# Kernel tuning notes

Measured on AMD Instinct MI355X. Metric: run time of the kernel, lower is better.

The kernel has to match this reference:

```python
import jax, jax.numpy as jnp
import numpy as np

B, C, S = 64, 512, 768          # batch, num_channels(seq), spatial_dim
K, K_NEXT, A, H = 128, 256, 200, 1024  # num_classes, next_num_classes, attention_unit, fc_hidden
BN_EPS = 1e-5


def setup_inputs() -> dict:
    key = jax.random.key(0)
    ks = jax.random.split(key, 8)
    return {
        "x": jax.random.normal(ks[0], (B, C, S), dtype=jnp.float32),
        "omega_h": jax.random.normal(ks[1], (B, K, A), dtype=jnp.float32),
        "W_s1": jax.random.normal(ks[2], (A, S), dtype=jnp.float32) * 0.1,
        "W_s2": jax.random.normal(ks[3], (K, A), dtype=jnp.float32) * 0.1,
        "W_t": jax.random.normal(ks[4], (H, 2 * S), dtype=jnp.float32) * 0.1,
        "b_t": jnp.full((H,), 0.1, dtype=jnp.float32),
        "gamma": jnp.ones((H,), dtype=jnp.float32),
        "beta": jnp.zeros((H,), dtype=jnp.float32),
        "W_l": jax.random.normal(ks[5], (K, H), dtype=jnp.float32) * 0.1,
        "b_l": jnp.full((K,), 0.1, dtype=jnp.float32),
        "G_h": jax.random.normal(ks[6], (K, K_NEXT), dtype=jnp.float32) * 0.1,
    }


def reference(x, omega_h, W_s1, W_s2, W_t, b_t, gamma, beta, W_l, b_l, G_h):
    # --- TCCA ---
    # tanh(W_s1 @ x^T): [B, A, C]
    t = jnp.tanh(jnp.einsum('as,bcs->bac', W_s1, x))
    # (W_s2 * omega_h) @ t : [B, K, C]
    attn = jnp.einsum('bka,bac->bkc', W_s2 * omega_h, t)
    attn_w = jax.nn.softmax(attn, axis=1)  # softmax over class dim (dim=1), as in source
    attn_out = jnp.einsum('bkc,bcs->bks', attn_w, x)
    attn_out_avg = jnp.mean(attn_out, axis=1)  # [B, S]

    # --- HAM concat ---
    x_mean = jnp.mean(x, axis=1)  # [B, S]
    local_input = jnp.concatenate([x_mean, attn_out_avg], axis=1)  # [B, 2S]

    # --- CPM: linear -> batchnorm(train) -> relu -> linear -> sigmoid ---
    fc = local_input @ W_t.T + b_t  # [B, H]
    mu = jnp.mean(fc, axis=0)
    var = jnp.mean(jnp.square(fc - mu), axis=0)  # biased variance (torch BN normalization)
    fc_bn = (fc - mu) * jax.lax.rsqrt(var + BN_EPS) * gamma + beta
    local_fc_out = jax.nn.relu(fc_bn)
    local_score = jax.nn.sigmoid(local_fc_out @ W_l.T + b_l)  # [B, K]

    # --- CDM ---
    Q_h = local_score @ G_h  # [B, K_NEXT]
    omega_h_next = jnp.broadcast_to(Q_h[:, :, None], (B, K_NEXT, A))

    return (local_score, local_fc_out, omega_h_next)
```

## Files before the change

kernel.cpp:

```cpp
#include <hip/hip_runtime.h>
#include <math.h>

#define B_  64
#define C_  512
#define S_  768
#define K_  128
#define KN_ 256
#define A_  200
#define H_  1024

#define OUT_FC     8192
#define OUT_OMEGA  73728

#define SCR_WEFF   0
#define SCR_XMT    786432
#define SCR_FCRT   835584
#define SCR_SCORET 901120

__global__ void __launch_bounds__(256) kA(const float* __restrict__ Wt,
                                          float* __restrict__ weff,
                                          const float* __restrict__ x,
                                          float* __restrict__ xmT) {
    __shared__ float4 smem[256];
    int tid = threadIdx.x;
    if (blockIdx.x < 768) {
        int idx = blockIdx.x * 256 + tid;
        int h   = idx / 192;
        int s4  = idx - h * 192;
        const float4* a = (const float4*)(Wt + (size_t)h * 1536) + s4;
        const float4* b = (const float4*)(Wt + (size_t)h * 1536 + 768) + s4;
        float4 va = *a, vb = *b;
        float4 r;
        r.x = va.x + 4.0f * vb.x;
        r.y = va.y + 4.0f * vb.y;
        r.z = va.z + 4.0f * vb.z;
        r.w = va.w + 4.0f * vb.w;
        ((float4*)weff)[idx] = r;
    } else {
        int bid = blockIdx.x - 768;
        int b   = bid / 12;
        int st  = (bid - b * 12) * 64;
        int s4  = tid & 15;
        int cs  = tid >> 4;
        const float4* xb = (const float4*)(x + (size_t)b * C_ * S_);
        int col = (st >> 2) + s4;
        float4 acc = {0.f, 0.f, 0.f, 0.f};
        #pragma unroll 8
        for (int c = cs; c < C_; c += 16) {
            float4 v = xb[c * 192 + col];
            acc.x += v.x; acc.y += v.y; acc.z += v.z; acc.w += v.w;
        }
        smem[tid] = acc;
        __syncthreads();
        #pragma unroll
        for (int str = 8; str >= 1; str >>= 1) {
            if (cs < str) {
                float4 o = smem[tid + str * 16];
                float4 m = smem[tid];
                m.x += o.x; m.y += o.y; m.z += o.z; m.w += o.w;
                smem[tid] = m;
            }
            __syncthreads();
        }
        if (cs == 0) {
            float4 m = smem[tid];
            const float inv = 1.0f / (float)C_;
            int scol = st + s4 * 4;
            xmT[(scol + 0) * 64 + b] = m.x * inv;
            xmT[(scol + 1) * 64 + b] = m.y * inv;
            xmT[(scol + 2) * 64 + b] = m.z * inv;
            xmT[(scol + 3) * 64 + b] = m.w * inv;
        }
    }
}

__global__ void __launch_bounds__(256) kB(const float* __restrict__ xmT,
                                          const float* __restrict__ weff,
                                          const float* __restrict__ bt,
                                          const float* __restrict__ gamma,
                                          const float* __restrict__ beta,
                                          float* __restrict__ fcrT,
                                          float* __restrict__ out_fc) {
    int lane = threadIdx.x & 63;
    int h = __builtin_amdgcn_readfirstlane((blockIdx.x << 2) + (threadIdx.x >> 6));
    const float4* w4 = (const float4*)(weff + (size_t)h * S_);
    float acc = 0.f;
    #pragma unroll 4
    for (int s4 = 0; s4 < 192; ++s4) {
        float4 w = w4[s4];
        int s = s4 * 4;
        acc += xmT[(s + 0) * 64 + lane] * w.x
             + xmT[(s + 1) * 64 + lane] * w.y
             + xmT[(s + 2) * 64 + lane] * w.z
             + xmT[(s + 3) * 64 + lane] * w.w;
    }
    float v = acc + bt[h];
    float s1 = v, s2 = v * v;
    #pragma unroll
    for (int m = 1; m < 64; m <<= 1) {
        s1 += __shfl_xor(s1, m);
        s2 += __shfl_xor(s2, m);
    }
    float mu  = s1 * (1.0f / 64.0f);
    float var = s2 * (1.0f / 64.0f) - mu * mu;
    float r = (v - mu) * rsqrtf(var + 1e-5f) * gamma[h] + beta[h];
    r = fmaxf(r, 0.0f);
    fcrT[h * 64 + lane]   = r;
    out_fc[lane * H_ + h] = r;
}

__global__ void __launch_bounds__(256) kC(const float* __restrict__ fcrT,
                                          const float* __restrict__ Wl,
                                          const float* __restrict__ bl,
                                          float* __restrict__ scoreT,
                                          float* __restrict__ out_score) {
    __shared__ float sm[256];
    int tid  = threadIdx.x;
    int lane = tid & 63;
    int w    = tid >> 6;
    int k    = blockIdx.x;
    const float* wl = Wl + (size_t)k * H_ + w * 256;
    const float* f  = fcrT + (size_t)w * 256 * 64;
    float acc = 0.f;
    #pragma unroll 8
    for (int h = 0; h < 256; ++h)
        acc += f[h * 64 + lane] * wl[h];
    sm[tid] = acc;
    __syncthreads();
    if (tid < 64) {
        float t = sm[tid] + sm[64 + tid] + sm[128 + tid] + sm[192 + tid] + bl[k];
        float sc = 1.0f / (1.0f + expf(-t));
        scoreT[k * 64 + tid]    = sc;
        out_score[tid * K_ + k] = sc;
    }
}

__global__ void __launch_bounds__(256) kD(const float* __restrict__ scoreT,
                                          const float* __restrict__ Gh,
                                          float4* __restrict__ outO) {
    __shared__ float qh[KN_];
    int tid = threadIdx.x;
    int b   = blockIdx.x >> 2;
    int q   = blockIdx.x & 3;
    float acc = 0.f;
    #pragma unroll 8
    for (int k = 0; k < K_; ++k)
        acc += scoreT[k * 64 + b] * Gh[k * KN_ + tid];
    qh[tid] = acc;
    __syncthreads();
    float4* dst = outO + (size_t)b * 12800;
    int end = q * 3200 + 3200;
    for (int i = q * 3200 + tid; i < end; i += 256) {
        float v = qh[i / 50];
        float4 r; r.x = v; r.y = v; r.z = v; r.w = v;
        dst[i] = r;
    }
}

extern "C" void kernel_launch(void* const* d_in, const int* in_sizes, int n_in,
                              void* d_out, int out_size, void* d_ws, size_t ws_size,
                              hipStream_t stream) {
    const float* x     = (const float*)d_in[0];
    const float* Wt    = (const float*)d_in[4];
    const float* bt    = (const float*)d_in[5];
    const float* gamma = (const float*)d_in[6];
    const float* beta  = (const float*)d_in[7];
    const float* Wl    = (const float*)d_in[8];
    const float* bl    = (const float*)d_in[9];
    const float* Gh    = (const float*)d_in[10];

    float* out    = (float*)d_out;
    float* ws     = (float*)d_ws;
    float* weff   = ws + SCR_WEFF;
    float* xmT    = ws + SCR_XMT;
    float* fcrT   = ws + SCR_FCRT;
    float* scoreT = ws + SCR_SCORET;

    kA<<<1536, 256, 0, stream>>>(Wt, weff, x, xmT);
    kB<<<256,  256, 0, stream>>>(xmT, weff, bt, gamma, beta, fcrT, out + OUT_FC);
    kC<<<128,  256, 0, stream>>>(fcrT, Wl, bl, scoreT, out);
    kD<<<256,  256, 0, stream>>>(scoreT, Gh, (float4*)(out + OUT_OMEGA));
}
```

Measured before the change: 219.5 us.

## Fuse weight folding into FC kernel and split reductions across more waves

The precomputed folded weight buffer (Wa + 4·Wb) is dropped. The FC kernel now reads both halves of W_t directly and combines them inline, which removes a full write and re-read of the folded weights from scratch memory along with the extra blocks in the first kernel. The FC kernel splits each hidden unit's reduction over the spatial dimension across two waves and merges them through shared memory. The score kernel moves to 512 threads so each wave handles a shorter slice of H. The cost is more raw W_t bytes read inside the FC kernel and an extra block barrier.

```diff
diff --git a/kernel.cpp b/kernel.cpp
--- a/kernel.cpp
+++ b/kernel.cpp
@@ -12,123 +12,119 @@
 #define OUT_FC     8192
 #define OUT_OMEGA  73728
 
-#define SCR_WEFF   0
-#define SCR_XMT    786432
-#define SCR_FCRT   835584
-#define SCR_SCORET 901120
+#define SCR_XMT    0
+#define SCR_FCRT   49152
+#define SCR_SCORET 114688
 
-__global__ void __launch_bounds__(256) kA(const float* __restrict__ Wt,
-                                          float* __restrict__ weff,
-                                          const float* __restrict__ x,
+__global__ void __launch_bounds__(256) kA(const float* __restrict__ x,
                                           float* __restrict__ xmT) {
     __shared__ float4 smem[256];
     int tid = threadIdx.x;
-    if (blockIdx.x < 768) {
-        int idx = blockIdx.x * 256 + tid;
-        int h   = idx / 192;
-        int s4  = idx - h * 192;
-        const float4* a = (const float4*)(Wt + (size_t)h * 1536) + s4;
-        const float4* b = (const float4*)(Wt + (size_t)h * 1536 + 768) + s4;
-        float4 va = *a, vb = *b;
-        float4 r;
-        r.x = va.x + 4.0f * vb.x;
-        r.y = va.y + 4.0f * vb.y;
-        r.z = va.z + 4.0f * vb.z;
-        r.w = va.w + 4.0f * vb.w;
-        ((float4*)weff)[idx] = r;
-    } else {
-        int bid = blockIdx.x - 768;
-        int b   = bid / 12;
-        int st  = (bid - b * 12) * 64;
-        int s4  = tid & 15;
-        int cs  = tid >> 4;
-        const float4* xb = (const float4*)(x + (size_t)b * C_ * S_);
-        int col = (st >> 2) + s4;
-        float4 acc = {0.f, 0.f, 0.f, 0.f};
-        #pragma unroll 8
-        for (int c = cs; c < C_; c += 16) {
-            float4 v = xb[c * 192 + col];
-            acc.x += v.x; acc.y += v.y; acc.z += v.z; acc.w += v.w;
+    int bid = blockIdx.x;
+    int b   = bid / 12;
+    int st  = (bid - b * 12) * 64;
+    int s4  = tid & 15;
+    int cs  = tid >> 4;
+    const float4* xb = (const float4*)(x + (size_t)b * C_ * S_);
+    int col = (st >> 2) + s4;
+    float4 acc = {0.f, 0.f, 0.f, 0.f};
+    #pragma unroll 8
+    for (int c = cs; c < C_; c += 16) {
+        float4 v = xb[c * 192 + col];
+        acc.x += v.x; acc.y += v.y; acc.z += v.z; acc.w += v.w;
+    }
+    smem[tid] = acc;
+    __syncthreads();
+    #pragma unroll
+    for (int str = 8; str >= 1; str >>= 1) {
+        if (cs < str) {
+            float4 o = smem[tid + str * 16];
+            float4 m = smem[tid];
+            m.x += o.x; m.y += o.y; m.z += o.z; m.w += o.w;
+            smem[tid] = m;
         }
-        smem[tid] = acc;
         __syncthreads();
-        #pragma unroll
-        for (int str = 8; str >= 1; str >>= 1) {
-            if (cs < str) {
-                float4 o = smem[tid + str * 16];
-                float4 m = smem[tid];
-                m.x += o.x; m.y += o.y; m.z += o.z; m.w += o.w;
-                smem[tid] = m;
-            }
-            __syncthreads();
-        }
-        if (cs == 0) {
-            float4 m = smem[tid];
-            const float inv = 1.0f / (float)C_;
-            int scol = st + s4 * 4;
-            xmT[(scol + 0) * 64 + b] = m.x * inv;
-            xmT[(scol + 1) * 64 + b] = m.y * inv;
-            xmT[(scol + 2) * 64 + b] = m.z * inv;
-            xmT[(scol + 3) * 64 + b] = m.w * inv;
-        }
+    }
+    if (cs == 0) {
+        float4 m = smem[tid];
+        const float inv = 1.0f / (float)C_;
+        int scol = st + s4 * 4;
+        xmT[(scol + 0) * 64 + b] = m.x * inv;
+        xmT[(scol + 1) * 64 + b] = m.y * inv;
+        xmT[(scol + 2) * 64 + b] = m.z * inv;
+        xmT[(scol + 3) * 64 + b] = m.w * inv;
     }
 }
 
 __global__ void __launch_bounds__(256) kB(const float* __restrict__ xmT,
-                                          const float* __restrict__ weff,
+                                          const float* __restrict__ Wt,
                                           const float* __restrict__ bt,
                                           const float* __restrict__ gamma,
                                           const float* __restrict__ beta,
                                           float* __restrict__ fcrT,
                                           float* __restrict__ out_fc) {
-    int lane = threadIdx.x & 63;
-    int h = __builtin_amdgcn_readfirstlane((blockIdx.x << 2) + (threadIdx.x >> 6));
-    const float4* w4 = (const float4*)(weff + (size_t)h * S_);
+    __shared__ float sm[4][64];
+    int tid  = threadIdx.x;
+    int lane = tid & 63;
+    int wid  = tid >> 6;
+    int hh   = wid >> 1;
+    int sh   = wid & 1;
+    int h    = __builtin_amdgcn_readfirstlane((blockIdx.x << 1) + hh);
+    const float4* wA = (const float4*)(Wt + (size_t)h * 1536) + sh * 96;
+    const float4* wB = (const float4*)(Wt + (size_t)h * 1536 + 768) + sh * 96;
+    const float*  xm = xmT + sh * 384 * 64;
     float acc = 0.f;
     #pragma unroll 4
-    for (int s4 = 0; s4 < 192; ++s4) {
-        float4 w = w4[s4];
-        int s = s4 * 4;
-        acc += xmT[(s + 0) * 64 + lane] * w.x
-             + xmT[(s + 1) * 64 + lane] * w.y
-             + xmT[(s + 2) * 64 + lane] * w.z
-             + xmT[(s + 3) * 64 + lane] * w.w;
+    for (int i = 0; i < 96; ++i) {
+        float4 a = wA[i], bq = wB[i];
+        int s = i * 4;
+        acc += xm[(s + 0) * 64 + lane] * (a.x + 4.0f * bq.x)
+             + xm[(s + 1) * 64 + lane] * (a.y + 4.0f * bq.y)
+             + xm[(s + 2) * 64 + lane] * (a.z + 4.0f * bq.z)
+             + xm[(s + 3) * 64 + lane] * (a.w + 4.0f * bq.w);
     }
-    float v = acc + bt[h];
-    float s1 = v, s2 = v * v;
-    #pragma unroll
-    for (int m = 1; m < 64; m <<= 1) {
-        s1 += __shfl_xor(s1, m);
-        s2 += __shfl_xor(s2, m);
+    sm[wid][lane] = acc;
+    __syncthreads();
+    if (wid < 2) {
+        int hg = __builtin_amdgcn_readfirstlane((blockIdx.x << 1) + wid);
+        float v = sm[2 * wid][lane] + sm[2 * wid + 1][lane] + bt[hg];
+        float s1 = v, s2 = v * v;
+        #pragma unroll
+        for (int m = 1; m < 64; m <<= 1) {
+            s1 += __shfl_xor(s1, m);
+            s2 += __shfl_xor(s2, m);
+        }
+        float mu  = s1 * (1.0f / 64.0f);
+        float var = s2 * (1.0f / 64.0f) - mu * mu;
+        float r = (v - mu) * rsqrtf(var + 1e-5f) * gamma[hg] + beta[hg];
+        r = fmaxf(r, 0.0f);
+        fcrT[hg * 64 + lane]   = r;
+        out_fc[lane * H_ + hg] = r;
     }
-    float mu  = s1 * (1.0f / 64.0f);
-    float var = s2 * (1.0f / 64.0f) - mu * mu;
-    float r = (v - mu) * rsqrtf(var + 1e-5f) * gamma[h] + beta[h];
-    r = fmaxf(r, 0.0f);
-    fcrT[h * 64 + lane]   = r;
-    out_fc[lane * H_ + h] = r;
 }
 
-__global__ void __launch_bounds__(256) kC(const float* __restrict__ fcrT,
+__global__ void __launch_bounds__(512) kC(const float* __restrict__ fcrT,
                                           const float* __restrict__ Wl,
                                           const float* __restrict__ bl,
                                           float* __restrict__ scoreT,
                                           float* __restrict__ out_score) {
-    __shared__ float sm[256];
+    __shared__ float sm[512];
     int tid  = threadIdx.x;
     int lane = tid & 63;
     int w    = tid >> 6;
     int k    = blockIdx.x;
-    const float* wl = Wl + (size_t)k * H_ + w * 256;
-    const float* f  = fcrT + (size_t)w * 256 * 64;
+    const float* wl = Wl + (size_t)k * H_ + w * 128;
+    const float* f  = fcrT + (size_t)w * 128 * 64;
     float acc = 0.f;
     #pragma unroll 8
-    for (int h = 0; h < 256; ++h)
+    for (int h = 0; h < 128; ++h)
         acc += f[h * 64 + lane] * wl[h];
     sm[tid] = acc;
     __syncthreads();
     if (tid < 64) {
-        float t = sm[tid] + sm[64 + tid] + sm[128 + tid] + sm[192 + tid] + bl[k];
+        float t = bl[k];
+        #pragma unroll
+        for (int j = 0; j < 8; ++j) t += sm[j * 64 + tid];
         float sc = 1.0f / (1.0f + expf(-t));
         scoreT[k * 64 + tid]    = sc;
         out_score[tid * K_ + k] = sc;
@@ -171,13 +167,12 @@
 
     float* out    = (float*)d_out;
     float* ws     = (float*)d_ws;
-    float* weff   = ws + SCR_WEFF;
     float* xmT    = ws + SCR_XMT;
     float* fcrT   = ws + SCR_FCRT;
     float* scoreT = ws + SCR_SCORET;
 
-    kA<<<1536, 256, 0, stream>>>(Wt, weff, x, xmT);
-    kB<<<256,  256, 0, stream>>>(xmT, weff, bt, gamma, beta, fcrT, out + OUT_FC);
-    kC<<<128,  256, 0, stream>>>(fcrT, Wl, bl, scoreT, out);
-    kD<<<256,  256, 0, stream>>>(scoreT, Gh, (float4*)(out + OUT_OMEGA));
+    kA<<<768, 256, 0, stream>>>(x, xmT);
+    kB<<<512, 256, 0, stream>>>(xmT, Wt, bt, gamma, beta, fcrT, out + OUT_FC);
+    kC<<<128, 512, 0, stream>>>(fcrT, Wl, bl, scoreT, out);
+    kD<<<256, 256, 0, stream>>>(scoreT, Gh, (float4*)(out + OUT_OMEGA));
 }
```

Measured after the change: 215.3 us. About the same (-1.9%).
